# Performance work log

Measured on AMD Instinct MI355X. Metric: run time of the kernel, lower is better.

The kernel has to match this reference:

```python
import jax, jax.numpy as jnp
import numpy as np

GAMMA = 1.0

def setup_inputs() -> dict:
    key = jax.random.key(0)
    k1, k2 = jax.random.split(key)
    N, D = 8192, 256
    X = jax.random.normal(k1, (N, D), dtype=jnp.float32)
    alpha_vec = jax.random.normal(k2, (N,), dtype=jnp.float32)
    return {"X": X, "alpha_vec": alpha_vec}

def reference(X, alpha_vec):
    sq = jnp.sum(X * X, axis=-1)                      # [N]
    d2 = sq[:, None] + sq[None, :] - 2.0 * (X @ X.T)  # [N, N]
    d2 = jnp.maximum(d2, 0.0)                         # guard tiny negatives
    K = jnp.exp(-GAMMA * d2)                          # RBF Gram matrix [N, N]
    return K @ alpha_vec                              # [N]
```

## Files before the change

kernel.cpp:

```cpp
#include <hip/hip_runtime.h>

typedef unsigned char u8;
typedef __attribute__((ext_vector_type(4))) float f32x4;
typedef __attribute__((ext_vector_type(4))) int i32x4;

#define RSTRIDE 264


__global__ void krr_prep8(const float* __restrict__ X, u8* __restrict__ Xb,
                          float* __restrict__ sq) {
    const int rl  = threadIdx.x >> 4;
    const int l   = threadIdx.x & 15;
    const int row = blockIdx.x * 16 + rl;
    const float* src = X + (size_t)row * 256 + l * 16;

    float s = 0.f;
    int wv[4];
    #pragma unroll
    for (int c = 0; c < 4; ++c) {
        int pk = __builtin_amdgcn_cvt_pk_fp8_f32(src[c*4+0], src[c*4+1], 0, false);
        pk     = __builtin_amdgcn_cvt_pk_fp8_f32(src[c*4+2], src[c*4+3], pk, true);
        wv[c] = pk;
        float x0 = __builtin_amdgcn_cvt_f32_fp8(pk, 0);
        float x1 = __builtin_amdgcn_cvt_f32_fp8(pk, 1);
        float x2 = __builtin_amdgcn_cvt_f32_fp8(pk, 2);
        float x3 = __builtin_amdgcn_cvt_f32_fp8(pk, 3);
        s = fmaf(x0, x0, s);
        s = fmaf(x1, x1, s);
        s = fmaf(x2, x2, s);
        s = fmaf(x3, x3, s);
    }
    *reinterpret_cast<i32x4*>(Xb + (size_t)row * 256 + l * 16) =
        (i32x4){wv[0], wv[1], wv[2], wv[3]};

    s += __shfl_xor(s, 1, 16);
    s += __shfl_xor(s, 2, 16);
    s += __shfl_xor(s, 4, 16);
    s += __shfl_xor(s, 8, 16);
    if (l == 0) sq[row] = s;
}


__global__ __launch_bounds__(1024) void krr_big(
    const u8* __restrict__ Xb, const float* __restrict__ sq,
    const float* __restrict__ alpha, float* __restrict__ P, int N)
{
    extern __shared__ __align__(16) u8 lds[];

    const int tid  = threadIdx.x;
    const int lane = tid & 63;
    const int w    = tid >> 6;
    const int wr   = (w >> 2) * 64;
    const int wc   = (w & 3) * 64;
    const int T    = N >> 8;
    const int nOff = T * (T - 1) / 2;

    int ti, tj;
    if ((int)blockIdx.x < nOff) {
        const int t = blockIdx.x;
        float Tf = (float)T - 0.5f;
        ti = (int)(Tf - sqrtf(fmaxf(Tf * Tf - 2.0f * (float)t, 0.f)));
        if (ti < 0) ti = 0;
        if (ti > T - 2) ti = T - 2;
        while ((ti + 1) * T - ((ti + 1) * (ti + 2)) / 2 <= t) ++ti;
        while (ti * T - (ti * (ti + 1)) / 2 > t) --ti;
        tj = ti + 1 + (t - (ti * T - (ti * (ti + 1)) / 2));
    } else {
        ti = tj = blockIdx.x - nOff;
    }
    const int rowBase = ti << 8;
    const int colBase = tj << 8;
    const bool offdiag = (ti != tj);

    {
        i32x4 regs[8];
        const int nit = offdiag ? 8 : 4;
        #pragma unroll
        for (int it = 0; it < 8; ++it) {
            if (it < nit) {
                int idx = it * 1024 + tid;
                int p   = idx >> 12;
                int r   = (idx >> 4) & 255;
                int c   = idx & 15;
                int gr  = (p ? colBase : rowBase) + r;
                regs[it] = *reinterpret_cast<const i32x4*>(&Xb[(size_t)gr * 256 + c * 16]);
            }
        }
        #pragma unroll
        for (int it = 0; it < 8; ++it) {
            if (it < nit) {
                int idx = it * 1024 + tid;
                int p   = idx >> 12;
                int r   = (idx >> 4) & 255;
                int c   = idx & 15;
                u8* dst = &lds[(size_t)(p * 256 + r) * RSTRIDE + c * 16];
                *reinterpret_cast<long*>(dst)     = ((const long*)&regs[it])[0];
                *reinterpret_cast<long*>(dst + 8) = ((const long*)&regs[it])[1];
            }
        }
    }
    __syncthreads();

    f32x4 acc[4][4];
    #pragma unroll
    for (int m = 0; m < 4; ++m)
        #pragma unroll
        for (int n = 0; n < 4; ++n)
            acc[m][n] = (f32x4){0.f, 0.f, 0.f, 0.f};

    const int g  = lane >> 4;
    const int rl = lane & 15;
    const u8* Abase = &lds[(size_t)(wr + rl) * RSTRIDE + g * 8];
    const u8* Bbase = &lds[(size_t)((offdiag ? 256 : 0) + wc + rl) * RSTRIDE + g * 8];

    #pragma unroll
    for (int ks = 0; ks < 8; ++ks) {
        long a[4], b[4];
        #pragma unroll
        for (int m = 0; m < 4; ++m)
            a[m] = *reinterpret_cast<const long*>(Abase + (size_t)m * 16 * RSTRIDE + ks * 32);
        #pragma unroll
        for (int n = 0; n < 4; ++n)
            b[n] = *reinterpret_cast<const long*>(Bbase + (size_t)n * 16 * RSTRIDE + ks * 32);
        #pragma unroll
        for (int m = 0; m < 4; ++m)
            #pragma unroll
            for (int n = 0; n < 4; ++n)
                acc[m][n] = __builtin_amdgcn_mfma_f32_16x16x32_fp8_fp8(
                    a[m], b[n], acc[m][n], 0, 0, 0);
    }

    float sqc[4], alc[4];
    #pragma unroll
    for (int n = 0; n < 4; ++n) {
        int c = colBase + wc + n * 16 + rl;
        sqc[n] = sq[c];
        alc[n] = alpha[c];
    }
    float csum[4] = {0.f, 0.f, 0.f, 0.f};
    float rowKeep[4] = {0.f, 0.f, 0.f, 0.f};
    #pragma unroll
    for (int m = 0; m < 4; ++m) {
        int r0 = rowBase + wr + m * 16 + g * 4;
        #pragma unroll
        for (int reg = 0; reg < 4; ++reg) {
            float sqr = sq[r0 + reg];
            float ar  = alpha[r0 + reg];
            float s = 0.f;
            #pragma unroll
            for (int n = 0; n < 4; ++n) {
                float d2 = sqr + sqc[n] - 2.0f * acc[m][n][reg];
                d2 = fmaxf(d2, 0.f);
                float k = __expf(-d2);
                s += k * alc[n];
                csum[n] = fmaf(k, ar, csum[n]);
            }
            s += __shfl_xor(s, 1, 16);
            s += __shfl_xor(s, 2, 16);
            s += __shfl_xor(s, 4, 16);
            s += __shfl_xor(s, 8, 16);
            if (reg == rl) rowKeep[m] = s;
        }
    }
    #pragma unroll
    for (int n = 0; n < 4; ++n) {
        csum[n] += __shfl_xor(csum[n], 16, 64);
        csum[n] += __shfl_xor(csum[n], 32, 64);
    }

    __syncthreads();
    float* ldsR = (float*)lds;
    float* ldsC = ldsR + 1024;
    if (rl < 4) {
        #pragma unroll
        for (int m = 0; m < 4; ++m)
            ldsR[(w & 3) * 256 + wr + m * 16 + g * 4 + rl] = rowKeep[m];
    }
    ldsC[(w >> 2) * 256 + wc + g * 16 + rl] = csum[g];
    __syncthreads();

    if (tid < 256) {
        float v = ldsR[tid] + ldsR[256 + tid] + ldsR[512 + tid] + ldsR[768 + tid];
        P[(size_t)tj * N + rowBase + tid] = v;
    } else if (tid < 512 && offdiag) {
        int r = tid - 256;
        float v = ldsC[r] + ldsC[256 + r] + ldsC[512 + r] + ldsC[768 + r];
        P[(size_t)ti * N + colBase + r] = v;
    }
}


__global__ void krr_reduce(const float* __restrict__ P, float* __restrict__ out,
                           int N, int T) {
    const int i = blockIdx.x * 256 + threadIdx.x;
    float s = 0.f;
    #pragma unroll 8
    for (int c = 0; c < T; ++c) s += P[(size_t)c * N + i];
    out[i] = s;
}


__global__ void krr_naive(const float* __restrict__ X, const float* __restrict__ alpha,
                          float* __restrict__ out, int N, int D) {
    __shared__ float xi[256];
    const int i = blockIdx.x;
    const int t = threadIdx.x;
    for (int k = t; k < D; k += blockDim.x) xi[k] = X[(size_t)i * D + k];
    __syncthreads();
    float s = 0.f;
    for (int j = t; j < N; j += blockDim.x) {
        float d2 = 0.f;
        const float* xj = &X[(size_t)j * D];
        for (int k = 0; k < D; ++k) {
            float d = xi[k] - xj[k];
            d2 = fmaf(d, d, d2);
        }
        s += __expf(-fmaxf(d2, 0.f)) * alpha[j];
    }
    #pragma unroll
    for (int off = 32; off > 0; off >>= 1) s += __shfl_xor(s, off, 64);
    __shared__ float red[4];
    const int lane = t & 63, w = t >> 6;
    if (lane == 0) red[w] = s;
    __syncthreads();
    if (t == 0) out[i] = red[0] + red[1] + red[2] + red[3];
}


extern "C" void kernel_launch(void* const* d_in, const int* in_sizes, int n_in,
                              void* d_out, int out_size, void* d_ws, size_t ws_size,
                              hipStream_t stream) {
    const float* X     = (const float*)d_in[0];
    const float* alpha = (const float*)d_in[1];
    float* out = (float*)d_out;

    const int N = in_sizes[1];
    const int D = in_sizes[0] / N;

    size_t xb_bytes = (size_t)N * D;
    size_t sq_bytes = (size_t)N * sizeof(float);
    const int T = N >> 8;
    size_t p_bytes  = (size_t)T * N * sizeof(float);
    size_t need     = xb_bytes + sq_bytes + p_bytes;

    const int ntiles = T * (T + 1) / 2;
    const size_t LDS_BYTES = (size_t)512 * RSTRIDE;

    bool shapes_ok = (D == 256) && (N % 256) == 0 && (N == out_size) && T >= 2;

    hipError_t e = hipFuncSetAttribute(
        reinterpret_cast<const void*>(krr_big),
        hipFuncAttributeMaxDynamicSharedMemorySize, (int)LDS_BYTES);

    if (ws_size >= need && shapes_ok && e == hipSuccess) {
        u8*    Xb = (u8*)d_ws;
        float* sq = (float*)((char*)d_ws + xb_bytes);
        float* P  = (float*)((char*)d_ws + xb_bytes + sq_bytes);
        krr_prep8<<<N / 16, 256, 0, stream>>>(X, Xb, sq);
        krr_big<<<ntiles, 1024, LDS_BYTES, stream>>>(Xb, sq, alpha, P, N);
        krr_reduce<<<N / 256, 256, 0, stream>>>(P, out, N, T);
    } else {
        (void)hipMemsetAsync(d_out, 0, (size_t)out_size * sizeof(float), stream);
        krr_naive<<<N, 256, 0, stream>>>(X, alpha, out, N, D);
    }
}
```

Baseline: 45.80 us.

## Persistent tile blocks with async global-to-LDS loads overlapped with epilogue

Replaces one-block-per-tile with a fixed grid of 256 persistent blocks, each processing 2 or 3 triangle tiles. The next tile is staged into LDS with global_load_lds while the exp/reduction epilogue of the current tile runs. It also swaps padded LDS rows for an XOR swizzle, cuts the row shuffle reduction by staging partials in LDS, and vectorises the final reduce with float4. The tile assignment is hardcoded for N=8192, so the fast path now requires that exact shape and is skipped for others.

Measured after the change: 64.52 us. +40.9%, slower.

```diff
diff --git a/kernel.cpp b/kernel.cpp
--- a/kernel.cpp
+++ b/kernel.cpp
@@ -4,7 +4,13 @@
 typedef __attribute__((ext_vector_type(4))) float f32x4;
 typedef __attribute__((ext_vector_type(4))) int i32x4;
 
-#define RSTRIDE 264
+
+__device__ __forceinline__ void gload_lds16(const void* g, void* l) {
+    __builtin_amdgcn_global_load_lds(
+        (const __attribute__((address_space(1))) void*)g,
+        (__attribute__((address_space(3))) void*)l,
+        16, 0, 0);
+}
 
 
 __global__ void krr_prep8(const float* __restrict__ X, u8* __restrict__ Xb,
@@ -41,12 +47,19 @@
 }
 
 
-__global__ __launch_bounds__(1024) void krr_big(
+#define LDS_ROWRED 131072
+#define LDS_COLRED 151552
+#define LDS_TOTAL  155648
+
+__global__ __launch_bounds__(1024) void krr_big2(
     const u8* __restrict__ Xb, const float* __restrict__ sq,
     const float* __restrict__ alpha, float* __restrict__ P, int N)
 {
     extern __shared__ __align__(16) u8 lds[];
-
+    float* rowredf = (float*)(lds + LDS_ROWRED);
+    float* colredf = (float*)(lds + LDS_COLRED);
+
+    const int bid  = blockIdx.x;
     const int tid  = threadIdx.x;
     const int lane = tid & 63;
     const int w    = tid >> 6;
@@ -55,148 +68,161 @@
     const int T    = N >> 8;
     const int nOff = T * (T - 1) / 2;
 
-    int ti, tj;
-    if ((int)blockIdx.x < nOff) {
-        const int t = blockIdx.x;
+    const int ntl = (bid < 240) ? 2 : 3;
+    auto tile_id = [&](int tt) {
+        return (bid < 240) ? (2 * bid + tt)
+                           : (tt == 0 ? 480 + (bid - 240)
+                                      : nOff + 2 * (bid - 240) + (tt - 1));
+    };
+
+    auto decode = [&](int t, int& rb, int& cb, bool& od) {
+        if (t >= nOff) { int d = t - nOff; rb = cb = d << 8; od = false; return; }
         float Tf = (float)T - 0.5f;
-        ti = (int)(Tf - sqrtf(fmaxf(Tf * Tf - 2.0f * (float)t, 0.f)));
+        int ti = (int)(Tf - sqrtf(fmaxf(Tf * Tf - 2.0f * (float)t, 0.f)));
         if (ti < 0) ti = 0;
         if (ti > T - 2) ti = T - 2;
         while ((ti + 1) * T - ((ti + 1) * (ti + 2)) / 2 <= t) ++ti;
         while (ti * T - (ti * (ti + 1)) / 2 > t) --ti;
-        tj = ti + 1 + (t - (ti * T - (ti * (ti + 1)) / 2));
-    } else {
-        ti = tj = blockIdx.x - nOff;
-    }
-    const int rowBase = ti << 8;
-    const int colBase = tj << 8;
-    const bool offdiag = (ti != tj);
-
-    {
-        i32x4 regs[8];
-        const int nit = offdiag ? 8 : 4;
-        #pragma unroll
-        for (int it = 0; it < 8; ++it) {
-            if (it < nit) {
+        int tj = ti + 1 + (t - (ti * T - (ti * (ti + 1)) / 2));
+        rb = ti << 8; cb = tj << 8; od = true;
+    };
+
+    auto stage = [&](int rb, int cb, bool od) {
+        #pragma unroll
+        for (int it = 0; it < 4; ++it) {
+            int idx = it * 1024 + tid;
+            int r = idx >> 4, c = idx & 15;
+            int gc = c ^ (r & 15);
+            gload_lds16(&Xb[(size_t)(rb + r) * 256 + gc * 16], &lds[idx * 16]);
+        }
+        if (od) {
+            #pragma unroll
+            for (int it = 0; it < 4; ++it) {
                 int idx = it * 1024 + tid;
-                int p   = idx >> 12;
-                int r   = (idx >> 4) & 255;
-                int c   = idx & 15;
-                int gr  = (p ? colBase : rowBase) + r;
-                regs[it] = *reinterpret_cast<const i32x4*>(&Xb[(size_t)gr * 256 + c * 16]);
-            }
-        }
-        #pragma unroll
-        for (int it = 0; it < 8; ++it) {
-            if (it < nit) {
-                int idx = it * 1024 + tid;
-                int p   = idx >> 12;
-                int r   = (idx >> 4) & 255;
-                int c   = idx & 15;
-                u8* dst = &lds[(size_t)(p * 256 + r) * RSTRIDE + c * 16];
-                *reinterpret_cast<long*>(dst)     = ((const long*)&regs[it])[0];
-                *reinterpret_cast<long*>(dst + 8) = ((const long*)&regs[it])[1];
-            }
-        }
-    }
+                int r = idx >> 4, c = idx & 15;
+                int gc = c ^ (r & 15);
+                gload_lds16(&Xb[(size_t)(cb + r) * 256 + gc * 16], &lds[65536 + idx * 16]);
+            }
+        }
+    };
+
+    const int cg = lane >> 4;
+    const int hh = cg & 1;
+    const int cs = cg >> 1;
+    const int rl = lane & 15;
+
+    int rb, cb; bool od;
+    decode(tile_id(0), rb, cb, od);
+    stage(rb, cb, od);
     __syncthreads();
 
-    f32x4 acc[4][4];
-    #pragma unroll
-    for (int m = 0; m < 4; ++m)
-        #pragma unroll
-        for (int n = 0; n < 4; ++n)
-            acc[m][n] = (f32x4){0.f, 0.f, 0.f, 0.f};
-
-    const int g  = lane >> 4;
-    const int rl = lane & 15;
-    const u8* Abase = &lds[(size_t)(wr + rl) * RSTRIDE + g * 8];
-    const u8* Bbase = &lds[(size_t)((offdiag ? 256 : 0) + wc + rl) * RSTRIDE + g * 8];
-
-    #pragma unroll
-    for (int ks = 0; ks < 8; ++ks) {
-        long a[4], b[4];
+    for (int tt = 0; tt < ntl; ++tt) {
+        const int bofs = od ? 65536 : 0;
+
+        f32x4 acc[4][4];
         #pragma unroll
         for (int m = 0; m < 4; ++m)
-            a[m] = *reinterpret_cast<const long*>(Abase + (size_t)m * 16 * RSTRIDE + ks * 32);
-        #pragma unroll
-        for (int n = 0; n < 4; ++n)
-            b[n] = *reinterpret_cast<const long*>(Bbase + (size_t)n * 16 * RSTRIDE + ks * 32);
-        #pragma unroll
-        for (int m = 0; m < 4; ++m)
             #pragma unroll
             for (int n = 0; n < 4; ++n)
-                acc[m][n] = __builtin_amdgcn_mfma_f32_16x16x32_fp8_fp8(
-                    a[m], b[n], acc[m][n], 0, 0, 0);
-    }
-
-    float sqc[4], alc[4];
-    #pragma unroll
-    for (int n = 0; n < 4; ++n) {
-        int c = colBase + wc + n * 16 + rl;
-        sqc[n] = sq[c];
-        alc[n] = alpha[c];
-    }
-    float csum[4] = {0.f, 0.f, 0.f, 0.f};
-    float rowKeep[4] = {0.f, 0.f, 0.f, 0.f};
-    #pragma unroll
-    for (int m = 0; m < 4; ++m) {
-        int r0 = rowBase + wr + m * 16 + g * 4;
-        #pragma unroll
-        for (int reg = 0; reg < 4; ++reg) {
-            float sqr = sq[r0 + reg];
-            float ar  = alpha[r0 + reg];
-            float s = 0.f;
+                acc[m][n] = (f32x4){0.f, 0.f, 0.f, 0.f};
+
+        #pragma unroll
+        for (int ks = 0; ks < 8; ++ks) {
+            const int ch = 2 * ks + cs;
+            long a[4], b[4];
+            #pragma unroll
+            for (int m = 0; m < 4; ++m) {
+                int r = wr + m * 16 + rl;
+                a[m] = *reinterpret_cast<const long*>(
+                    &lds[r * 256 + ((ch ^ (r & 15)) << 4) + hh * 8]);
+            }
             #pragma unroll
             for (int n = 0; n < 4; ++n) {
-                float d2 = sqr + sqc[n] - 2.0f * acc[m][n][reg];
-                d2 = fmaxf(d2, 0.f);
-                float k = __expf(-d2);
-                s += k * alc[n];
-                csum[n] = fmaf(k, ar, csum[n]);
-            }
-            s += __shfl_xor(s, 1, 16);
-            s += __shfl_xor(s, 2, 16);
-            s += __shfl_xor(s, 4, 16);
-            s += __shfl_xor(s, 8, 16);
-            if (reg == rl) rowKeep[m] = s;
-        }
-    }
-    #pragma unroll
-    for (int n = 0; n < 4; ++n) {
-        csum[n] += __shfl_xor(csum[n], 16, 64);
-        csum[n] += __shfl_xor(csum[n], 32, 64);
-    }
-
-    __syncthreads();
-    float* ldsR = (float*)lds;
-    float* ldsC = ldsR + 1024;
-    if (rl < 4) {
-        #pragma unroll
-        for (int m = 0; m < 4; ++m)
-            ldsR[(w & 3) * 256 + wr + m * 16 + g * 4 + rl] = rowKeep[m];
-    }
-    ldsC[(w >> 2) * 256 + wc + g * 16 + rl] = csum[g];
-    __syncthreads();
-
-    if (tid < 256) {
-        float v = ldsR[tid] + ldsR[256 + tid] + ldsR[512 + tid] + ldsR[768 + tid];
-        P[(size_t)tj * N + rowBase + tid] = v;
-    } else if (tid < 512 && offdiag) {
-        int r = tid - 256;
-        float v = ldsC[r] + ldsC[256 + r] + ldsC[512 + r] + ldsC[768 + r];
-        P[(size_t)ti * N + colBase + r] = v;
-    }
-}
-
-
-__global__ void krr_reduce(const float* __restrict__ P, float* __restrict__ out,
-                           int N, int T) {
+                int r = wc + n * 16 + rl;
+                b[n] = *reinterpret_cast<const long*>(
+                    &lds[bofs + r * 256 + ((ch ^ (r & 15)) << 4) + hh * 8]);
+            }
+            #pragma unroll
+            for (int m = 0; m < 4; ++m)
+                #pragma unroll
+                for (int n = 0; n < 4; ++n)
+                    acc[m][n] = __builtin_amdgcn_mfma_f32_16x16x32_fp8_fp8(
+                        a[m], b[n], acc[m][n], 0, 0, 0);
+        }
+        __syncthreads();
+
+        int rb2 = 0, cb2 = 0; bool od2 = false;
+        if (tt + 1 < ntl) {
+            decode(tile_id(tt + 1), rb2, cb2, od2);
+            stage(rb2, cb2, od2);
+        }
+
+        float sqc[4], alc[4];
+        #pragma unroll
+        for (int n = 0; n < 4; ++n) {
+            int c = cb + wc + n * 16 + rl;
+            sqc[n] = sq[c];
+            alc[n] = alpha[c];
+        }
+        float csum[4] = {0.f, 0.f, 0.f, 0.f};
+        #pragma unroll
+        for (int m = 0; m < 4; ++m) {
+            int r0 = rb + wr + m * 16 + cg * 4;
+            #pragma unroll
+            for (int reg = 0; reg < 4; ++reg) {
+                float sqr = sq[r0 + reg];
+                float ar  = alpha[r0 + reg];
+                float s = 0.f;
+                #pragma unroll
+                for (int n = 0; n < 4; ++n) {
+                    float d2 = sqr + sqc[n] - 2.0f * acc[m][n][reg];
+                    d2 = fmaxf(d2, 0.f);
+                    float k = __expf(-d2);
+                    s += k * alc[n];
+                    csum[n] = fmaf(k, ar, csum[n]);
+                }
+                s += __shfl_xor(s, 1, 16);
+                s += __shfl_xor(s, 2, 16);
+                if ((rl & 3) == reg) {
+                    int lrow = wr + m * 16 + cg * 4 + reg;
+                    rowredf[((w & 3) * 256 + lrow) * 5 + (rl >> 2)] = s;
+                }
+            }
+        }
+        #pragma unroll
+        for (int n = 0; n < 4; ++n) {
+            csum[n] += __shfl_xor(csum[n], 16);
+            csum[n] += __shfl_xor(csum[n], 32);
+            if (cg == 0)
+                colredf[(w >> 2) * 256 + wc + n * 16 + rl] = csum[n];
+        }
+        __syncthreads();
+
+        if (tid < 256) {
+            float v = 0.f;
+            #pragma unroll
+            for (int wcg = 0; wcg < 4; ++wcg)
+                #pragma unroll
+                for (int q = 0; q < 4; ++q)
+                    v += rowredf[(wcg * 256 + tid) * 5 + q];
+            P[(size_t)(cb >> 8) * N + rb + tid] = v;
+        } else if (tid < 512 && od) {
+            int c = tid - 256;
+            float v = colredf[c] + colredf[256 + c] + colredf[512 + c] + colredf[768 + c];
+            P[(size_t)(rb >> 8) * N + cb + c] = v;
+        }
+
+        rb = rb2; cb = cb2; od = od2;
+    }
+}
+
+
+__global__ void krr_reduce(const f32x4* __restrict__ Pv, f32x4* __restrict__ outv,
+                           int nvec, int T) {
     const int i = blockIdx.x * 256 + threadIdx.x;
-    float s = 0.f;
-    #pragma unroll 8
-    for (int c = 0; c < T; ++c) s += P[(size_t)c * N + i];
-    out[i] = s;
+    f32x4 s = (f32x4){0.f, 0.f, 0.f, 0.f};
+    for (int c = 0; c < T; ++c) s += Pv[(size_t)c * nvec + i];
+    outv[i] = s;
 }
 
 
@@ -243,22 +269,19 @@
     size_t p_bytes  = (size_t)T * N * sizeof(float);
     size_t need     = xb_bytes + sq_bytes + p_bytes;
 
-    const int ntiles = T * (T + 1) / 2;
-    const size_t LDS_BYTES = (size_t)512 * RSTRIDE;
-
-    bool shapes_ok = (D == 256) && (N % 256) == 0 && (N == out_size) && T >= 2;
+    bool shapes_ok = (D == 256) && (N == 8192) && (N == out_size);
 
     hipError_t e = hipFuncSetAttribute(
-        reinterpret_cast<const void*>(krr_big),
-        hipFuncAttributeMaxDynamicSharedMemorySize, (int)LDS_BYTES);
+        reinterpret_cast<const void*>(krr_big2),
+        hipFuncAttributeMaxDynamicSharedMemorySize, LDS_TOTAL);
 
     if (ws_size >= need && shapes_ok && e == hipSuccess) {
         u8*    Xb = (u8*)d_ws;
         float* sq = (float*)((char*)d_ws + xb_bytes);
         float* P  = (float*)((char*)d_ws + xb_bytes + sq_bytes);
         krr_prep8<<<N / 16, 256, 0, stream>>>(X, Xb, sq);
-        krr_big<<<ntiles, 1024, LDS_BYTES, stream>>>(Xb, sq, alpha, P, N);
-        krr_reduce<<<N / 256, 256, 0, stream>>>(P, out, N, T);
+        krr_big2<<<256, 1024, LDS_TOTAL, stream>>>(Xb, sq, alpha, P, N);
+        krr_reduce<<<N / 1024, 256, 0, stream>>>((const f32x4*)P, (f32x4*)out, N / 4, T);
     } else {
         (void)hipMemsetAsync(d_out, 0, (size_t)out_size * sizeof(float), stream);
         krr_naive<<<N, 256, 0, stream>>>(X, alpha, out, N, D);
```
